# Optimization experiments

Measured on AMD Instinct MI355X. Metric: run time of the kernel, lower is better.

The kernel has to match this reference:

```python
import jax, jax.numpy as jnp
import numpy as np

N_NODES = 100000
N_HYPEREDGES = 30000
N_INC = 300000
IN_CH = 128
HID = 256
OUT_CH = 128
EPS = 1e-5


def setup_inputs() -> dict:
    key = jax.random.key(0)
    ks = jax.random.split(key, 14)
    x = jax.random.normal(ks[0], (N_NODES, IN_CH), jnp.float32)
    node_idx = jax.random.randint(ks[1], (N_INC,), 0, N_NODES)
    he_idx = jax.random.randint(ks[2], (N_INC,), 0, N_HYPEREDGES)
    edge = jnp.stack([node_idx, he_idx], axis=0)  # [2, N_INC]
    s1 = 1.0 / np.sqrt(IN_CH)
    s2 = 1.0 / np.sqrt(HID)
    return {
        "x": x,
        "edge": edge,
        "W1": jax.random.normal(ks[3], (IN_CH, HID), jnp.float32) * s1,
        "b1": jnp.zeros((HID,), jnp.float32),
        "g1": jnp.ones((HID,), jnp.float32),
        "be1": jnp.zeros((HID,), jnp.float32),
        "W2": jax.random.normal(ks[4], (HID, HID), jnp.float32) * s2,
        "b2": jnp.zeros((HID,), jnp.float32),
        "g2": jnp.ones((HID,), jnp.float32),
        "be2": jnp.zeros((HID,), jnp.float32),
        "W3": jax.random.normal(ks[5], (HID, OUT_CH), jnp.float32) * s2,
        "b3": jnp.zeros((OUT_CH,), jnp.float32),
    }


def _hconv(x, node_idx, he_idx, W, b):
    # PyG HypergraphConv (no attention, unit hyperedge weights):
    # X' = D^{-1} H B^{-1} H^T (X @ W) + b
    x = x @ W  # [N, F]
    ones = jnp.ones((node_idx.shape[0],), x.dtype)
    d = jax.ops.segment_sum(ones, node_idx, num_segments=N_NODES)       # node degree
    bd = jax.ops.segment_sum(ones, he_idx, num_segments=N_HYPEREDGES)  # hyperedge degree
    Dinv = jnp.where(d > 0, 1.0 / jnp.maximum(d, 1.0), 0.0)
    Binv = jnp.where(bd > 0, 1.0 / jnp.maximum(bd, 1.0), 0.0)
    # node -> hyperedge aggregation, scaled by B^{-1}
    he = jax.ops.segment_sum(x[node_idx], he_idx, num_segments=N_HYPEREDGES) * Binv[:, None]
    # hyperedge -> node aggregation, scaled by D^{-1}
    out = jax.ops.segment_sum(he[he_idx], node_idx, num_segments=N_NODES) * Dinv[:, None]
    return out + b


def _bn(x, g, be):
    # BatchNorm1d, training mode (batch statistics over nodes)
    m = x.mean(axis=0)
    v = x.var(axis=0)
    return (x - m) * jax.lax.rsqrt(v + EPS) * g + be


def reference(x, edge, W1, b1, g1, be1, W2, b2, g2, be2, W3, b3):
    node_idx = edge[0]
    he_idx = edge[1]
    h = _bn(jax.nn.relu(_hconv(x, node_idx, he_idx, W1, b1)), g1, be1)
    h = _bn(jax.nn.relu(_hconv(h, node_idx, he_idx, W2, b2)), g2, be2)
    h = jax.nn.relu(_hconv(h, node_idx, he_idx, W3, b3))
    return h
```

## Files before the change

kernel.cpp:

```cpp
#include <hip/hip_runtime.h>

#define N_NODES 100000
#define N_HE    30000
#define N_INC   300000
#define HEPAD   30080

typedef short  short8  __attribute__((ext_vector_type(8)));
typedef float  floatx4 __attribute__((ext_vector_type(4)));

__device__ inline unsigned short f2bf(float f) {
  unsigned int u = __float_as_uint(f);
  u = (u + 0x7fff + ((u >> 16) & 1)) >> 16;
  return (unsigned short)u;
}
__device__ inline unsigned int pack2(float lo, float hi) {
  return (unsigned int)f2bf(lo) | ((unsigned int)f2bf(hi) << 16);
}
__device__ inline void acc8(uint4 rv, float* a) {
  unsigned int u;
  u = rv.x; a[0] += __uint_as_float(u << 16); a[1] += __uint_as_float(u & 0xffff0000u);
  u = rv.y; a[2] += __uint_as_float(u << 16); a[3] += __uint_as_float(u & 0xffff0000u);
  u = rv.z; a[4] += __uint_as_float(u << 16); a[5] += __uint_as_float(u & 0xffff0000u);
  u = rv.w; a[6] += __uint_as_float(u << 16); a[7] += __uint_as_float(u & 0xffff0000u);
}

__device__ inline void gather4(const unsigned short* __restrict__ base,
                               const int* __restrict__ idx, int beg, int end,
                               int F, int c0, float* a) {
  for (int j = beg; j < end; j += 4) {
    int d = end - j;
    int j1 = j + (d > 1 ? 1 : 0);
    int j2 = j + (d > 2 ? 2 : 0);
    int j3 = j + (d > 3 ? 3 : 0);
    int e0 = idx[j], e1 = idx[j1], e2 = idx[j2], e3 = idx[j3];
    uint4 r0 = *(const uint4*)(base + (size_t)e0 * F + c0);
    uint4 r1 = *(const uint4*)(base + (size_t)e1 * F + c0);
    uint4 r2 = *(const uint4*)(base + (size_t)e2 * F + c0);
    uint4 r3 = *(const uint4*)(base + (size_t)e3 * F + c0);
    acc8(r0, a);
    if (d > 1) acc8(r1, a);
    if (d > 2) acc8(r2, a);
    if (d > 3) acc8(r3, a);
  }
}


__global__ void zero_kernel(int* __restrict__ p, int n) {
  int i = blockIdx.x * blockDim.x + threadIdx.x;
  if (i < n) p[i] = 0;
}

__global__ void count_kernel(const int* __restrict__ nidx, const int* __restrict__ hidx,
                             int* __restrict__ node_cnt, int* __restrict__ he_cnt) {
  int i = blockIdx.x * blockDim.x + threadIdx.x;
  if (i < N_INC) {
    atomicAdd(&node_cnt[nidx[i]], 1);
    atomicAdd(&he_cnt[hidx[i]], 1);
  }
}

__global__ void scan1(const int* __restrict__ cnt, int* __restrict__ incl,
                      int* __restrict__ bsums, int n) {
  __shared__ int tmp[1024];
  int tid = threadIdx.x;
  int i = blockIdx.x * 1024 + tid;
  tmp[tid] = (i < n) ? cnt[i] : 0;
  __syncthreads();
  for (int off = 1; off < 1024; off <<= 1) {
    int t = (tid >= off) ? tmp[tid - off] : 0;
    __syncthreads();
    tmp[tid] += t;
    __syncthreads();
  }
  if (i < n) incl[i] = tmp[tid];
  if (tid == 1023) bsums[blockIdx.x] = tmp[1023];
}

__global__ void scan2(int* __restrict__ bsums, int nb) {
  if (threadIdx.x == 0 && blockIdx.x == 0) {
    int run = 0;
    for (int b = 0; b < nb; b++) { int v = bsums[b]; bsums[b] = run; run += v; }
  }
}

__global__ void scan3(const int* __restrict__ cnt, const int* __restrict__ incl,
                      const int* __restrict__ bsums, int* __restrict__ ptr,
                      int* __restrict__ fill, int n) {
  int i = blockIdx.x * 1024 + threadIdx.x;
  if (i < n) {
    int e = incl[i] - cnt[i] + bsums[blockIdx.x];
    ptr[i] = e;
    fill[i] = e;
    if (i == n - 1) ptr[n] = incl[i] + bsums[blockIdx.x];
  }
}

__global__ void fill_kernel(const int* __restrict__ nidx, const int* __restrict__ hidx,
                            int* __restrict__ node_fill, int* __restrict__ he_fill,
                            int* __restrict__ node_hes, int* __restrict__ he_nodes) {
  int i = blockIdx.x * blockDim.x + threadIdx.x;
  if (i < N_INC) {
    int nn = nidx[i], hh = hidx[i];
    int p1 = atomicAdd(&node_fill[nn], 1);
    node_hes[p1] = hh;
    int p2 = atomicAdd(&he_fill[hh], 1);
    he_nodes[p2] = nn;
  }
}


__global__ void convert_x(const float* __restrict__ x, unsigned short* __restrict__ xb) {
  int i = blockIdx.x * 256 + threadIdx.x;
  if (i >= N_NODES * 16) return;
  const float4* p = (const float4*)x + (size_t)i * 2;
  float4 a = p[0], b = p[1];
  uint4 o;
  o.x = pack2(a.x, a.y); o.y = pack2(a.z, a.w);
  o.z = pack2(b.x, b.y); o.w = pack2(b.z, b.w);
  *(uint4*)(xb + (size_t)i * 8) = o;
}

__global__ __launch_bounds__(256) void fold_w(
    const float* __restrict__ W, const float* __restrict__ scale,
    const float* __restrict__ shift, unsigned short* __restrict__ WT,
    float* __restrict__ cvec, int K, int N) {
  int n = blockIdx.y * 256 + threadIdx.x;
  if (n >= N) return;
  int k0 = blockIdx.x * 16;
  float c = 0.f;
  unsigned short loc[16];
#pragma unroll
  for (int i = 0; i < 16; i++) {
    int k = k0 + i;
    float w = W[(size_t)k * N + n];
    float s = scale ? scale[k] : 1.f;
    float t = shift ? shift[k] : 0.f;
    loc[i] = f2bf(w * s);
    c += t * w;
  }
  *(uint4*)(WT + (size_t)n * K + k0)     = *(const uint4*)&loc[0];
  *(uint4*)(WT + (size_t)n * K + k0 + 8) = *(const uint4*)&loc[8];
  atomicAdd(cvec + n, c);
}

__global__ void bn_finalize(const float* __restrict__ gsum, const float* __restrict__ gss,
                            const float* __restrict__ g, const float* __restrict__ be,
                            float* __restrict__ scale, float* __restrict__ shift, float invN) {
  int c = threadIdx.x;
  float m = gsum[c] * invN;
  float v = gss[c] * invN - m * m;
  float sc = g[c] * rsqrtf(v + 1e-5f);
  scale[c] = sc;
  shift[c] = be[c] - m * sc;
}


__global__ __launch_bounds__(256) void gemm_mfma(
    const unsigned short* __restrict__ A, const unsigned short* __restrict__ BT,
    unsigned short* __restrict__ C, int K, int N) {
  __shared__ unsigned short As[128 * 32];
  __shared__ unsigned short Bs[128 * 32];
  const int tid  = threadIdx.x;
  const int w    = tid >> 6, lane = tid & 63;
  const int wm   = w & 1,  wn   = w >> 1;
  const int bm   = blockIdx.x * 128, bn = blockIdx.y * 128;
  const int quad = lane >> 4, r16 = lane & 15;

  floatx4 acc[4][4] = {};

  const int srow = (lane >> 2);
  const int scol = (lane & 3) * 8;

  for (int kb = 0; kb < K; kb += 32) {
#pragma unroll
    for (int i = 0; i < 2; i++) {
      const int row = (w * 2 + i) * 16 + srow;
      const unsigned short* ga = A  + (size_t)(bm + row) * K + kb + scol;
      const unsigned short* gb = BT + (size_t)(bn + row) * K + kb + scol;
      __builtin_amdgcn_global_load_lds(
          (const __attribute__((address_space(1))) void*)ga,
          (__attribute__((address_space(3))) void*)(&As[(w * 2 + i) * 512]), 16, 0, 0);
      __builtin_amdgcn_global_load_lds(
          (const __attribute__((address_space(1))) void*)gb,
          (__attribute__((address_space(3))) void*)(&Bs[(w * 2 + i) * 512]), 16, 0, 0);
    }
    __syncthreads();
    short8 af[4], bfr[4];
#pragma unroll
    for (int t = 0; t < 4; t++) {
      af[t]  = *(const short8*)&As[(wm * 64 + t * 16 + r16) * 32 + quad * 8];
      bfr[t] = *(const short8*)&Bs[(wn * 64 + t * 16 + r16) * 32 + quad * 8];
    }
#pragma unroll
    for (int mi = 0; mi < 4; mi++)
#pragma unroll
      for (int ni = 0; ni < 4; ni++)
        acc[mi][ni] = __builtin_amdgcn_mfma_f32_16x16x32_bf16(af[mi], bfr[ni], acc[mi][ni], 0, 0, 0);
    __syncthreads();
  }
#pragma unroll
  for (int mi = 0; mi < 4; mi++)
#pragma unroll
    for (int ni = 0; ni < 4; ni++)
#pragma unroll
      for (int rr = 0; rr < 4; rr++) {
        int gm = bm + wm * 64 + mi * 16 + quad * 4 + rr;
        int gn = bn + wn * 64 + ni * 16 + r16;
        C[(size_t)gm * N + gn] = f2bf(acc[mi][ni][rr]);
      }
}


__global__ __launch_bounds__(256) void agg_he(
    const unsigned short* __restrict__ src, const int* __restrict__ ptr,
    const int* __restrict__ idx, unsigned short* __restrict__ dst,
    int F, int shift, int nSeg) {
  int seg = blockIdx.x * (256 >> shift) + (threadIdx.x >> shift);
  if (seg >= nSeg) return;
  int l = threadIdx.x & ((1 << shift) - 1);
  int c0 = l * 8;
  int beg = ptr[seg], end = ptr[seg + 1];
  float a[8] = {};
  gather4(src, idx, beg, end, F, c0, a);
  float inv = (end > beg) ? 1.0f / (float)(end - beg) : 0.0f;
  uint4 o;
  o.x = pack2(a[0] * inv, a[1] * inv);
  o.y = pack2(a[2] * inv, a[3] * inv);
  o.z = pack2(a[4] * inv, a[5] * inv);
  o.w = pack2(a[6] * inv, a[7] * inv);
  *(uint4*)(dst + (size_t)seg * F + c0) = o;
}

__global__ __launch_bounds__(256) void node_agg_bn(
    const unsigned short* __restrict__ he, const int* __restrict__ nptr,
    const int* __restrict__ nhes, const float* __restrict__ b,
    const float* __restrict__ cvec, unsigned short* __restrict__ dst,
    float* __restrict__ gsum, float* __restrict__ gss) {
  const int F = 256;
  const int grp = threadIdx.x >> 5, l = threadIdx.x & 31, c0 = l * 8;
  float bb[8], cc[8];
#pragma unroll
  for (int j = 0; j < 8; j++) { bb[j] = b[c0 + j]; cc[j] = cvec[c0 + j]; }
  float s[8] = {}, ss[8] = {};
  for (int i = 0; i < 8; i++) {
    int n = blockIdx.x * 64 + i * 8 + grp;
    if (n >= N_NODES) continue;
    int beg = nptr[n], end = nptr[n + 1];
    float a[8] = {};
    gather4(he, nhes, beg, end, F, c0, a);
    float inv = (end > beg) ? 1.0f / (float)(end - beg) : 0.0f;
    float cmul = (end > beg) ? 1.0f : 0.0f;
    float o[8];
#pragma unroll
    for (int j = 0; j < 8; j++) {
      o[j] = fmaxf(fmaf(a[j], inv, bb[j] + cmul * cc[j]), 0.f);
      s[j] += o[j]; ss[j] += o[j] * o[j];
    }
    uint4 ov;
    ov.x = pack2(o[0], o[1]); ov.y = pack2(o[2], o[3]);
    ov.z = pack2(o[4], o[5]); ov.w = pack2(o[6], o[7]);
    *(uint4*)(dst + (size_t)n * F + c0) = ov;
  }
  __shared__ float Ls[8][256];
  __shared__ float Lss[8][256];
#pragma unroll
  for (int j = 0; j < 8; j++) { Ls[grp][c0 + j] = s[j]; Lss[grp][c0 + j] = ss[j]; }
  __syncthreads();
  int c = threadIdx.x;
  float a1 = 0.f, a2 = 0.f;
#pragma unroll
  for (int h = 0; h < 8; h++) { a1 += Ls[h][c]; a2 += Lss[h][c]; }
  atomicAdd(gsum + c, a1);
  atomicAdd(gss + c, a2);
}

__global__ __launch_bounds__(256) void agg_out(
    const unsigned short* __restrict__ he, const int* __restrict__ nptr,
    const int* __restrict__ nhes, const float* __restrict__ b,
    const float* __restrict__ cvec, float* __restrict__ out) {
  const int F = 128;
  int g = threadIdx.x >> 4, l = threadIdx.x & 15, c0 = l * 8;
  int n = blockIdx.x * 16 + g;
  if (n >= N_NODES) return;
  int beg = nptr[n], end = nptr[n + 1];
  float a[8] = {};
  gather4(he, nhes, beg, end, F, c0, a);
  float inv = (end > beg) ? 1.0f / (float)(end - beg) : 0.0f;
  float cmul = (end > beg) ? 1.0f : 0.0f;
  float4 o0, o1;
  o0.x = fmaxf(fmaf(a[0], inv, b[c0 + 0] + cmul * cvec[c0 + 0]), 0.f);
  o0.y = fmaxf(fmaf(a[1], inv, b[c0 + 1] + cmul * cvec[c0 + 1]), 0.f);
  o0.z = fmaxf(fmaf(a[2], inv, b[c0 + 2] + cmul * cvec[c0 + 2]), 0.f);
  o0.w = fmaxf(fmaf(a[3], inv, b[c0 + 3] + cmul * cvec[c0 + 3]), 0.f);
  o1.x = fmaxf(fmaf(a[4], inv, b[c0 + 4] + cmul * cvec[c0 + 4]), 0.f);
  o1.y = fmaxf(fmaf(a[5], inv, b[c0 + 5] + cmul * cvec[c0 + 5]), 0.f);
  o1.z = fmaxf(fmaf(a[6], inv, b[c0 + 6] + cmul * cvec[c0 + 6]), 0.f);
  o1.w = fmaxf(fmaf(a[7], inv, b[c0 + 7] + cmul * cvec[c0 + 7]), 0.f);
  float* dp = out + (size_t)n * F + c0;
  *(float4*)dp = o0;
  *(float4*)(dp + 4) = o1;
}


extern "C" void kernel_launch(void* const* d_in, const int* in_sizes, int n_in,
                              void* d_out, int out_size, void* d_ws, size_t ws_size,
                              hipStream_t stream) {
  const float* x    = (const float*)d_in[0];
  const int*   edge = (const int*)d_in[1];
  const int*   nidx = edge;
  const int*   hidx = edge + N_INC;
  const float* W1  = (const float*)d_in[2];
  const float* b1  = (const float*)d_in[3];
  const float* g1  = (const float*)d_in[4];
  const float* be1 = (const float*)d_in[5];
  const float* W2  = (const float*)d_in[6];
  const float* b2  = (const float*)d_in[7];
  const float* g2  = (const float*)d_in[8];
  const float* be2 = (const float*)d_in[9];
  const float* W3  = (const float*)d_in[10];
  const float* b3  = (const float*)d_in[11];
  float* out = (float*)d_out;

  char* ws = (char*)d_ws;
  size_t off = 0;
  auto alloc = [&](size_t bytes) -> void* {
    void* p = ws + off;
    off = (off + bytes + 255) & ~(size_t)255;
    return p;
  };
  unsigned short* Xb   = (unsigned short*)alloc((size_t)N_NODES * 128 * 2);
  unsigned short* Bb   = (unsigned short*)alloc((size_t)N_NODES * 256 * 2);
  unsigned short* Hraw = (unsigned short*)alloc((size_t)HEPAD * 256 * 2);
  unsigned short* HEb  = (unsigned short*)alloc((size_t)HEPAD * 256 * 2);
  unsigned short* W1T  = (unsigned short*)alloc((size_t)256 * 128 * 2);
  unsigned short* W2T  = (unsigned short*)alloc((size_t)256 * 256 * 2);
  unsigned short* W3T  = (unsigned short*)alloc((size_t)128 * 256 * 2);
  size_t zero_begin = off;
  int* he_cnt   = (int*)alloc((size_t)N_HE * 4);
  int* node_cnt = (int*)alloc((size_t)N_NODES * 4);
  float* gsum1 = (float*)alloc(1024);
  float* gss1  = (float*)alloc(1024);
  float* gsum2 = (float*)alloc(1024);
  float* gss2  = (float*)alloc(1024);
  float* c1 = (float*)alloc(1024);
  float* c2 = (float*)alloc(1024);
  float* c3 = (float*)alloc(1024);
  size_t zero_end = off;
  int* he_ptr    = (int*)alloc((size_t)(N_HE + 1) * 4);
  int* node_ptr  = (int*)alloc((size_t)(N_NODES + 1) * 4);
  int* he_fill   = (int*)alloc((size_t)N_HE * 4);
  int* node_fill = (int*)alloc((size_t)N_NODES * 4);
  int* he_nodes  = (int*)alloc((size_t)N_INC * 4);
  int* node_hes  = (int*)alloc((size_t)N_INC * 4);
  int* incl      = (int*)alloc((size_t)N_NODES * 4);
  int* bsums     = (int*)alloc(512);
  float* scale1 = (float*)alloc(1024);
  float* shift1 = (float*)alloc(1024);
  float* scale2 = (float*)alloc(1024);
  float* shift2 = (float*)alloc(1024);

  int zero_ints = (int)((zero_end - zero_begin) / 4);
  zero_kernel<<<(zero_ints + 255) / 256, 256, 0, stream>>>(he_cnt, zero_ints);
  count_kernel<<<(N_INC + 255) / 256, 256, 0, stream>>>(nidx, hidx, node_cnt, he_cnt);
  {
    int nb = (N_HE + 1023) / 1024;
    scan1<<<nb, 1024, 0, stream>>>(he_cnt, incl, bsums, N_HE);
    scan2<<<1, 64, 0, stream>>>(bsums, nb);
    scan3<<<nb, 1024, 0, stream>>>(he_cnt, incl, bsums, he_ptr, he_fill, N_HE);
  }
  {
    int nb = (N_NODES + 1023) / 1024;
    scan1<<<nb, 1024, 0, stream>>>(node_cnt, incl, bsums, N_NODES);
    scan2<<<1, 64, 0, stream>>>(bsums, nb);
    scan3<<<nb, 1024, 0, stream>>>(node_cnt, incl, bsums, node_ptr, node_fill, N_NODES);
  }
  fill_kernel<<<(N_INC + 255) / 256, 256, 0, stream>>>(nidx, hidx, node_fill, he_fill,
                                                       node_hes, he_nodes);

  convert_x<<<(N_NODES * 16 + 255) / 256, 256, 0, stream>>>(x, Xb);
  { dim3 g(128 / 16, 1); fold_w<<<g, 256, 0, stream>>>(W1, nullptr, nullptr, W1T, c1, 128, 256); }

  const int MBHE = HEPAD / 128;
  const float invN = 1.0f / (float)N_NODES;

  agg_he<<<(N_HE + 15) / 16, 256, 0, stream>>>(Xb, he_ptr, he_nodes, Hraw, 128, 4, N_HE);
  { dim3 g(MBHE, 2); gemm_mfma<<<g, 256, 0, stream>>>(Hraw, W1T, HEb, 128, 256); }
  node_agg_bn<<<(N_NODES + 63) / 64, 256, 0, stream>>>(HEb, node_ptr, node_hes, b1, c1,
                                                       Bb, gsum1, gss1);
  bn_finalize<<<1, 256, 0, stream>>>(gsum1, gss1, g1, be1, scale1, shift1, invN);

  { dim3 g(256 / 16, 1); fold_w<<<g, 256, 0, stream>>>(W2, scale1, shift1, W2T, c2, 256, 256); }
  agg_he<<<(N_HE + 7) / 8, 256, 0, stream>>>(Bb, he_ptr, he_nodes, Hraw, 256, 5, N_HE);
  { dim3 g(MBHE, 2); gemm_mfma<<<g, 256, 0, stream>>>(Hraw, W2T, HEb, 256, 256); }
  node_agg_bn<<<(N_NODES + 63) / 64, 256, 0, stream>>>(HEb, node_ptr, node_hes, b2, c2,
                                                       Bb, gsum2, gss2);
  bn_finalize<<<1, 256, 0, stream>>>(gsum2, gss2, g2, be2, scale2, shift2, invN);

  { dim3 g(256 / 16, 1); fold_w<<<g, 256, 0, stream>>>(W3, scale2, shift2, W3T, c3, 256, 128); }
  agg_he<<<(N_HE + 7) / 8, 256, 0, stream>>>(Bb, he_ptr, he_nodes, Hraw, 256, 5, N_HE);
  { dim3 g(MBHE, 1); gemm_mfma<<<g, 256, 0, stream>>>(Hraw, W3T, HEb, 256, 128); }
  agg_out<<<(N_NODES + 15) / 16, 256, 0, stream>>>(HEb, node_ptr, node_hes, b3, c3, out);
}
```

Measured before the change: 474.9 us.

## Prefetch gather indices eight-wide and fold BN finalize into weight folding

Swaps the 4-wide gather loop for an 8-wide one that prefetches the next batch of indices while the current rows load. In node_agg_bn, the index loads for the next node are issued before the current node's rows are accumulated, which hides index-load latency. The separate bn_finalize kernels are removed and their statistics math is done inside fold_w, and the zero kernel becomes a hipMemsetAsync, cutting the launch count. The wider gathers raise register use and load redundant clamped rows when the degree is small.

```diff
diff --git a/kernel.cpp b/kernel.cpp
--- a/kernel.cpp
+++ b/kernel.cpp
@@ -24,31 +24,44 @@
   u = rv.w; a[6] += __uint_as_float(u << 16); a[7] += __uint_as_float(u & 0xffff0000u);
 }
 
-__device__ inline void gather4(const unsigned short* __restrict__ base,
-                               const int* __restrict__ idx, int beg, int end,
-                               int F, int c0, float* a) {
-  for (int j = beg; j < end; j += 4) {
-    int d = end - j;
-    int j1 = j + (d > 1 ? 1 : 0);
-    int j2 = j + (d > 2 ? 2 : 0);
-    int j3 = j + (d > 3 ? 3 : 0);
-    int e0 = idx[j], e1 = idx[j1], e2 = idx[j2], e3 = idx[j3];
-    uint4 r0 = *(const uint4*)(base + (size_t)e0 * F + c0);
-    uint4 r1 = *(const uint4*)(base + (size_t)e1 * F + c0);
-    uint4 r2 = *(const uint4*)(base + (size_t)e2 * F + c0);
-    uint4 r3 = *(const uint4*)(base + (size_t)e3 * F + c0);
-    acc8(r0, a);
-    if (d > 1) acc8(r1, a);
-    if (d > 2) acc8(r2, a);
-    if (d > 3) acc8(r3, a);
-  }
-}
-
-
-__global__ void zero_kernel(int* __restrict__ p, int n) {
-  int i = blockIdx.x * blockDim.x + threadIdx.x;
-  if (i < n) p[i] = 0;
-}
+struct R8 { uint4 r[8]; };
+
+__device__ inline void load8(const unsigned short* __restrict__ base, const int* e,
+                             int F, int c0, R8& o) {
+#pragma unroll
+  for (int k = 0; k < 8; k++)
+    o.r[k] = *(const uint4*)(base + (size_t)e[k] * F + c0);
+}
+__device__ inline void accm8(const R8& o, int d, float* a) {
+  acc8(o.r[0], a);
+  if (d > 1) acc8(o.r[1], a);
+  if (d > 2) acc8(o.r[2], a);
+  if (d > 3) acc8(o.r[3], a);
+  if (d > 4) acc8(o.r[4], a);
+  if (d > 5) acc8(o.r[5], a);
+  if (d > 6) acc8(o.r[6], a);
+  if (d > 7) acc8(o.r[7], a);
+}
+
+__device__ inline void gather8p(const unsigned short* __restrict__ base,
+                                const int* __restrict__ idx, int beg, int end,
+                                int F, int c0, float* a) {
+  if (beg >= end) return;
+  int e[8];
+#pragma unroll
+  for (int k = 0; k < 8; k++) e[k] = idx[min(beg + k, end - 1)];
+  for (int j = beg; j < end; j += 8) {
+    R8 r;
+    load8(base, e, F, c0, r);
+    int jn = j + 8;
+    if (jn < end) {
+#pragma unroll
+      for (int k = 0; k < 8; k++) e[k] = idx[min(jn + k, end - 1)];
+    }
+    accm8(r, end - j, a);
+  }
+}
+
 
 __global__ void count_kernel(const int* __restrict__ nidx, const int* __restrict__ hidx,
                              int* __restrict__ node_cnt, int* __restrict__ he_cnt) {
@@ -121,9 +134,10 @@
 }
 
 __global__ __launch_bounds__(256) void fold_w(
-    const float* __restrict__ W, const float* __restrict__ scale,
-    const float* __restrict__ shift, unsigned short* __restrict__ WT,
-    float* __restrict__ cvec, int K, int N) {
+    const float* __restrict__ W, const float* __restrict__ gsum,
+    const float* __restrict__ gss, const float* __restrict__ g,
+    const float* __restrict__ be, unsigned short* __restrict__ WT,
+    float* __restrict__ cvec, int K, int N, float invN) {
   int n = blockIdx.y * 256 + threadIdx.x;
   if (n >= N) return;
   int k0 = blockIdx.x * 16;
@@ -133,25 +147,19 @@
   for (int i = 0; i < 16; i++) {
     int k = k0 + i;
     float w = W[(size_t)k * N + n];
-    float s = scale ? scale[k] : 1.f;
-    float t = shift ? shift[k] : 0.f;
+    float s = 1.f, t = 0.f;
+    if (gsum) {
+      float m = gsum[k] * invN;
+      float v = gss[k] * invN - m * m;
+      s = g[k] * rsqrtf(v + 1e-5f);
+      t = be[k] - m * s;
+    }
     loc[i] = f2bf(w * s);
     c += t * w;
   }
   *(uint4*)(WT + (size_t)n * K + k0)     = *(const uint4*)&loc[0];
   *(uint4*)(WT + (size_t)n * K + k0 + 8) = *(const uint4*)&loc[8];
   atomicAdd(cvec + n, c);
-}
-
-__global__ void bn_finalize(const float* __restrict__ gsum, const float* __restrict__ gss,
-                            const float* __restrict__ g, const float* __restrict__ be,
-                            float* __restrict__ scale, float* __restrict__ shift, float invN) {
-  int c = threadIdx.x;
-  float m = gsum[c] * invN;
-  float v = gss[c] * invN - m * m;
-  float sc = g[c] * rsqrtf(v + 1e-5f);
-  scale[c] = sc;
-  shift[c] = be[c] - m * sc;
 }
 
 
@@ -221,7 +229,7 @@
   int c0 = l * 8;
   int beg = ptr[seg], end = ptr[seg + 1];
   float a[8] = {};
-  gather4(src, idx, beg, end, F, c0, a);
+  gather8p(src, idx, beg, end, F, c0, a);
   float inv = (end > beg) ? 1.0f / (float)(end - beg) : 0.0f;
   uint4 o;
   o.x = pack2(a[0] * inv, a[1] * inv);
@@ -241,25 +249,56 @@
   float bb[8], cc[8];
 #pragma unroll
   for (int j = 0; j < 8; j++) { bb[j] = b[c0 + j]; cc[j] = cvec[c0 + j]; }
-  float s[8] = {}, ss[8] = {};
+  int begs[8], ends[8];
+#pragma unroll
   for (int i = 0; i < 8; i++) {
     int n = blockIdx.x * 64 + i * 8 + grp;
-    if (n >= N_NODES) continue;
-    int beg = nptr[n], end = nptr[n + 1];
+    begs[i] = (n < N_NODES) ? nptr[n] : 0;
+    ends[i] = (n < N_NODES) ? nptr[n + 1] : 0;
+  }
+  float s[8] = {}, ss[8] = {};
+  int e[8];
+#pragma unroll
+  for (int k = 0; k < 8; k++)
+    e[k] = (begs[0] < ends[0]) ? nhes[min(begs[0] + k, ends[0] - 1)] : 0;
+  for (int i = 0; i < 8; i++) {
+    const int beg = begs[i], end = ends[i];
+    const int d = end - beg;
+    const int n = blockIdx.x * 64 + i * 8 + grp;
     float a[8] = {};
-    gather4(he, nhes, beg, end, F, c0, a);
-    float inv = (end > beg) ? 1.0f / (float)(end - beg) : 0.0f;
-    float cmul = (end > beg) ? 1.0f : 0.0f;
-    float o[8];
-#pragma unroll
-    for (int j = 0; j < 8; j++) {
-      o[j] = fmaxf(fmaf(a[j], inv, bb[j] + cmul * cc[j]), 0.f);
-      s[j] += o[j]; ss[j] += o[j] * o[j];
-    }
-    uint4 ov;
-    ov.x = pack2(o[0], o[1]); ov.y = pack2(o[2], o[3]);
-    ov.z = pack2(o[4], o[5]); ov.w = pack2(o[6], o[7]);
-    *(uint4*)(dst + (size_t)n * F + c0) = ov;
+    R8 r;
+    if (d > 0) load8(he, e, F, c0, r);
+    if (i < 7) {
+      int bn2 = begs[i + 1], en2 = ends[i + 1];
+#pragma unroll
+      for (int k = 0; k < 8; k++)
+        e[k] = (bn2 < en2) ? nhes[min(bn2 + k, en2 - 1)] : 0;
+    }
+    if (d > 0) {
+      accm8(r, d, a);
+      for (int j = beg + 8; j < end; j += 8) {
+        int et[8];
+#pragma unroll
+        for (int k = 0; k < 8; k++) et[k] = nhes[min(j + k, end - 1)];
+        R8 t;
+        load8(he, et, F, c0, t);
+        accm8(t, end - j, a);
+      }
+    }
+    if (n < N_NODES) {
+      float inv  = (d > 0) ? 1.0f / (float)d : 0.0f;
+      float cmul = (d > 0) ? 1.0f : 0.0f;
+      float o[8];
+#pragma unroll
+      for (int j = 0; j < 8; j++) {
+        o[j] = fmaxf(fmaf(a[j], inv, bb[j] + cmul * cc[j]), 0.f);
+        s[j] += o[j]; ss[j] += o[j] * o[j];
+      }
+      uint4 ov;
+      ov.x = pack2(o[0], o[1]); ov.y = pack2(o[2], o[3]);
+      ov.z = pack2(o[4], o[5]); ov.w = pack2(o[6], o[7]);
+      *(uint4*)(dst + (size_t)n * F + c0) = ov;
+    }
   }
   __shared__ float Ls[8][256];
   __shared__ float Lss[8][256];
@@ -284,7 +323,7 @@
   if (n >= N_NODES) return;
   int beg = nptr[n], end = nptr[n + 1];
   float a[8] = {};
-  gather4(he, nhes, beg, end, F, c0, a);
+  gather8p(he, nhes, beg, end, F, c0, a);
   float inv = (end > beg) ? 1.0f / (float)(end - beg) : 0.0f;
   float cmul = (end > beg) ? 1.0f : 0.0f;
   float4 o0, o1;
@@ -354,13 +393,9 @@
   int* node_hes  = (int*)alloc((size_t)N_INC * 4);
   int* incl      = (int*)alloc((size_t)N_NODES * 4);
   int* bsums     = (int*)alloc(512);
-  float* scale1 = (float*)alloc(1024);
-  float* shift1 = (float*)alloc(1024);
-  float* scale2 = (float*)alloc(1024);
-  float* shift2 = (float*)alloc(1024);
-
-  int zero_ints = (int)((zero_end - zero_begin) / 4);
-  zero_kernel<<<(zero_ints + 255) / 256, 256, 0, stream>>>(he_cnt, zero_ints);
+
+  hipMemsetAsync((void*)(ws + zero_begin), 0, zero_end - zero_begin, stream);
+
   count_kernel<<<(N_INC + 255) / 256, 256, 0, stream>>>(nidx, hidx, node_cnt, he_cnt);
   {
     int nb = (N_HE + 1023) / 1024;
@@ -378,7 +413,8 @@
                                                        node_hes, he_nodes);
 
   convert_x<<<(N_NODES * 16 + 255) / 256, 256, 0, stream>>>(x, Xb);
-  { dim3 g(128 / 16, 1); fold_w<<<g, 256, 0, stream>>>(W1, nullptr, nullptr, W1T, c1, 128, 256); }
+  { dim3 g(128 / 16, 1);
+    fold_w<<<g, 256, 0, stream>>>(W1, nullptr, nullptr, nullptr, nullptr, W1T, c1, 128, 256, 0.f); }
 
   const int MBHE = HEPAD / 128;
   const float invN = 1.0f / (float)N_NODES;
@@ -387,16 +423,16 @@
   { dim3 g(MBHE, 2); gemm_mfma<<<g, 256, 0, stream>>>(Hraw, W1T, HEb, 128, 256); }
   node_agg_bn<<<(N_NODES + 63) / 64, 256, 0, stream>>>(HEb, node_ptr, node_hes, b1, c1,
                                                        Bb, gsum1, gss1);
-  bn_finalize<<<1, 256, 0, stream>>>(gsum1, gss1, g1, be1, scale1, shift1, invN);
-
-  { dim3 g(256 / 16, 1); fold_w<<<g, 256, 0, stream>>>(W2, scale1, shift1, W2T, c2, 256, 256); }
+
+  { dim3 g(256 / 16, 1);
+    fold_w<<<g, 256, 0, stream>>>(W2, gsum1, gss1, g1, be1, W2T, c2, 256, 256, invN); }
   agg_he<<<(N_HE + 7) / 8, 256, 0, stream>>>(Bb, he_ptr, he_nodes, Hraw, 256, 5, N_HE);
   { dim3 g(MBHE, 2); gemm_mfma<<<g, 256, 0, stream>>>(Hraw, W2T, HEb, 256, 256); }
   node_agg_bn<<<(N_NODES + 63) / 64, 256, 0, stream>>>(HEb, node_ptr, node_hes, b2, c2,
                                                        Bb, gsum2, gss2);
-  bn_finalize<<<1, 256, 0, stream>>>(gsum2, gss2, g2, be2, scale2, shift2, invN);
-
-  { dim3 g(256 / 16, 1); fold_w<<<g, 256, 0, stream>>>(W3, scale2, shift2, W3T, c3, 256, 128); }
+
+  { dim3 g(256 / 16, 1);
+    fold_w<<<g, 256, 0, stream>>>(W3, gsum2, gss2, g2, be2, W3T, c3, 256, 128, invN); }
   agg_he<<<(N_HE + 7) / 8, 256, 0, stream>>>(Bb, he_ptr, he_nodes, Hraw, 256, 5, N_HE);
   { dim3 g(MBHE, 1); gemm_mfma<<<g, 256, 0, stream>>>(Hraw, W3T, HEb, 256, 128); }
   agg_out<<<(N_NODES + 15) / 16, 256, 0, stream>>>(HEb, node_ptr, node_hes, b3, c3, out);
```

New measurement: 450.8 us. -5.1%, faster.
